# Kernel tuning notes

Measured on AMD Instinct MI355X. Metric: run time of the kernel, lower is better.

The kernel has to match this reference:

```python
import jax, jax.numpy as jnp
import numpy as np

N_NODES = 50000
N_EDGES = 800000


def _gcn_norm(edge_index, n_nodes):
    # add self-loops, compute symmetric normalization D^-1/2 (A+I) D^-1/2
    loops = jnp.arange(n_nodes, dtype=edge_index.dtype)
    row = jnp.concatenate([edge_index[0], loops])
    col = jnp.concatenate([edge_index[1], loops])
    deg = jax.ops.segment_sum(jnp.ones_like(row, dtype=jnp.float32), row,
                              num_segments=n_nodes)
    dinv = jnp.where(deg > 0, jax.lax.rsqrt(deg), 0.0)
    norm = dinv[row] * dinv[col]  # [E+N]
    return row, col, norm


def _gcn_conv(x, W, b, row, col, norm, n_nodes):
    h = x @ W                                  # [N, out] transform first (cheaper gather)
    msg = norm[:, None] * h[col]               # [E+N, out]
    agg = jax.ops.segment_sum(msg, row, num_segments=n_nodes)
    return agg + b


def setup_inputs() -> dict:
    key = jax.random.key(0)
    ks = jax.random.split(key, 8)
    F_in, H, F_out = 64, 128, 64
    return {
        "features": jax.random.normal(ks[0], (N_NODES, F_in), jnp.float32),
        "W1": jax.random.normal(ks[1], (F_in, H), jnp.float32) / np.sqrt(F_in),
        "b1": jnp.zeros((H,), jnp.float32),
        "W2": jax.random.normal(ks[2], (H, H), jnp.float32) / np.sqrt(H),
        "b2": jnp.zeros((H,), jnp.float32),
        "W3": jax.random.normal(ks[3], (H, F_out), jnp.float32) / np.sqrt(H),
        "b3": jnp.zeros((F_out,), jnp.float32),
        "edge_index": jax.random.randint(ks[4], (2, N_EDGES), 0, N_NODES, jnp.int32),
    }


def reference(features, W1, b1, W2, b2, W3, b3, edge_index):
    n = features.shape[0]
    row, col, norm = _gcn_norm(edge_index, n)
    x = jax.nn.relu(_gcn_conv(features, W1, b1, row, col, norm, n))
    x = jax.nn.relu(_gcn_conv(x, W2, b2, row, col, norm, n))
    x = _gcn_conv(x, W3, b3, row, col, norm, n)
    return x
```

## Files before the change

### kernel.cpp

```cpp
#include <hip/hip_runtime.h>

#define N_NODES 50000
#define N_EDGES 800000

#define SCAN_CHUNK 256
#define SCAN_BLOCKS ((N_NODES + SCAN_CHUNK - 1) / SCAN_CHUNK)

static inline size_t alignUp(size_t x, size_t a) { return (x + a - 1) & ~(a - 1); }

typedef _Float16 h2 __attribute__((ext_vector_type(2)));
typedef _Float16 h4 __attribute__((ext_vector_type(4)));
typedef _Float16 h8 __attribute__((ext_vector_type(8)));
typedef float    f4 __attribute__((ext_vector_type(4)));


__global__ void k_zero_i32(int* __restrict__ p, int n) {
    int i = blockIdx.x * 256 + threadIdx.x;
    if (i < n) p[i] = 0;
}

__global__ void k_count4(const int* __restrict__ row, int* __restrict__ count,
                         int* __restrict__ rank, int* __restrict__ pad) {
    int i = blockIdx.x * 256 + threadIdx.x;
    if (i < 64) pad[i] = 0;
    if (i < N_EDGES / 4) {
        int4 r = reinterpret_cast<const int4*>(row)[i];
        int k0 = atomicAdd(&count[r.x], 1);
        int k1 = atomicAdd(&count[r.y], 1);
        int k2 = atomicAdd(&count[r.z], 1);
        int k3 = atomicAdd(&count[r.w], 1);
        reinterpret_cast<int4*>(rank)[i] = make_int4(k0, k1, k2, k3);
    }
}

__global__ void k_blocksum(const int* __restrict__ count, int* __restrict__ bsum) {
    __shared__ int s[256];
    int t = threadIdx.x;
    int i = blockIdx.x * 256 + t;
    int v = (i < N_NODES) ? count[i] : 0;
    s[t] = v;
    __syncthreads();
    for (int off = 128; off > 0; off >>= 1) {
        if (t < off) s[t] += s[t + off];
        __syncthreads();
    }
    if (t == 0) bsum[blockIdx.x] = s[0];
}

__global__ void k_scan_bsum(int* __restrict__ bsum) {
    __shared__ int s[256];
    int t = threadIdx.x;
    int v = (t < SCAN_BLOCKS) ? bsum[t] : 0;
    s[t] = v;
    __syncthreads();
    for (int off = 1; off < 256; off <<= 1) {
        int add = (t >= off) ? s[t - off] : 0;
        __syncthreads();
        s[t] += add;
        __syncthreads();
    }
    if (t < SCAN_BLOCKS) bsum[t] = s[t] - v;
}

__global__ void k_scan_final(const int* __restrict__ count, const int* __restrict__ bsum,
                             int* __restrict__ offsets, float* __restrict__ dinv) {
    __shared__ int s[256];
    int t = threadIdx.x;
    int i = blockIdx.x * 256 + t;
    int v = (i < N_NODES) ? count[i] : 0;
    s[t] = v;
    __syncthreads();
    for (int off = 1; off < 256; off <<= 1) {
        int add = (t >= off) ? s[t - off] : 0;
        __syncthreads();
        s[t] += add;
        __syncthreads();
    }
    if (i < N_NODES) {
        offsets[i] = s[t] - v + bsum[blockIdx.x];
        dinv[i]    = rsqrtf((float)(v + 1));
    }
}

__global__ void k_scatter(const int* __restrict__ row, const int* __restrict__ col,
                          const int* __restrict__ offsets, const int* __restrict__ rank,
                          int* __restrict__ csr_col,
                          const float* __restrict__ feat, const float* __restrict__ dinv,
                          _Float16* __restrict__ featS) {
    int e = blockIdx.x * 256 + threadIdx.x;
    if (e < N_EDGES) {
        int node = e >> 4;
        float d = dinv[node];
        float4 v = reinterpret_cast<const float4*>(feat)[e];
        h4 hv = {(_Float16)(v.x * d), (_Float16)(v.y * d),
                 (_Float16)(v.z * d), (_Float16)(v.w * d)};
        reinterpret_cast<h4*>(featS)[e] = hv;
        int r = row[e];
        csr_col[offsets[r] + rank[e]] = col[e];
    }
}


__global__ void k_prepw(const float* __restrict__ W1, const float* __restrict__ W2,
                        const float* __restrict__ W3, _Float16* __restrict__ W1T,
                        _Float16* __restrict__ W2T, _Float16* __restrict__ W3T) {
    int i = blockIdx.x * 256 + threadIdx.x;
    if (i < 8192) {
        int n = i >> 6, k = i & 63;
        W1T[i] = (_Float16)W1[k * 128 + n];
    } else if (i < 24576) {
        int j = i - 8192; int n = j >> 7, k = j & 127;
        W2T[j] = (_Float16)W2[k * 128 + n];
    } else {
        int j = i - 24576; int n = j >> 7, k = j & 127;
        W3T[j] = (_Float16)W3[k * 64 + n];
    }
}


template <bool BIAS, bool HOUT>
__global__ __launch_bounds__(256) void k_agg128(const _Float16* __restrict__ hs, void* __restrict__ out,
        const int* __restrict__ csr_col, const int* __restrict__ offsets,
        const int* __restrict__ count, const float* __restrict__ dinv,
        const float* __restrict__ bias) {
    int lane = threadIdx.x & 63;
    int node = blockIdx.x * 4 + (threadIdx.x >> 6);
    const char* base = (const char*)hs;
    uint32_t lo = (uint32_t)lane << 2;

    float ax[8], ay[8];
#pragma unroll
    for (int u = 0; u < 8; u++) { ax[u] = 0.f; ay[u] = 0.f; }

    int n = count[node];
    const int* cp = csr_col + offsets[node];

    int e = 0;
    for (; e + 8 <= n; e += 8) {
        int c[8];
#pragma unroll
        for (int u = 0; u < 8; u++) c[u] = cp[e + u];
#pragma unroll
        for (int u = 0; u < 8; u++) {
            h2 v = *reinterpret_cast<const h2*>(base + (((uint32_t)c[u] << 8) + lo));
            ax[u] += (float)v.x; ay[u] += (float)v.y;
        }
    }
    if (e < n) {
        int c[8];
#pragma unroll
        for (int u = 0; u < 8; u++) c[u] = cp[e + u];
#pragma unroll
        for (int u = 0; u < 8; u++) {
            h2 v = *reinterpret_cast<const h2*>(base + (((uint32_t)c[u] << 8) + lo));
            if (e + u < n) { ax[u] += (float)v.x; ay[u] += (float)v.y; }
        }
    }

    float sx = 0.f, sy = 0.f;
#pragma unroll
    for (int u = 0; u < 8; u++) { sx += ax[u]; sy += ay[u]; }
    h2 self = *reinterpret_cast<const h2*>(base + (((uint32_t)node << 8) + lo));
    float d = dinv[node];
    float ox = (sx + (float)self.x) * d, oy = (sy + (float)self.y) * d;
    if (BIAS) { ox += bias[2 * lane]; oy += bias[2 * lane + 1]; }
    if constexpr (HOUT) {
        h2 hv = {(_Float16)ox, (_Float16)oy};
        reinterpret_cast<h2*>(out)[(size_t)node * 64 + lane] = hv;
    } else {
        reinterpret_cast<float2*>(out)[(size_t)node * 64 + lane] = make_float2(ox, oy);
    }
}

template <bool BIAS, bool HOUT>
__global__ __launch_bounds__(256) void k_agg64(const _Float16* __restrict__ hs, void* __restrict__ out,
        const int* __restrict__ csr_col, const int* __restrict__ offsets,
        const int* __restrict__ count, const float* __restrict__ dinv,
        const float* __restrict__ bias) {
    int lane = threadIdx.x & 63;
    int node = blockIdx.x * 4 + (threadIdx.x >> 6);
    int q = lane >> 4;
    int f4 = lane & 15;
    const char* base = (const char*)hs;
    uint32_t fo = (uint32_t)f4 << 3;

    int n = __builtin_amdgcn_readfirstlane(count[node]);
    int start = __builtin_amdgcn_readfirstlane(offsets[node]);
    const int* cp = csr_col + start;

    float4 a0 = make_float4(0.f, 0.f, 0.f, 0.f);
    float4 a1 = make_float4(0.f, 0.f, 0.f, 0.f);

    int e = 0;
    for (; e + 32 <= n; e += 32) {
        int c[8];
#pragma unroll
        for (int u = 0; u < 8; u++) c[u] = cp[e + 4 * u + q];
        h4 v[8];
#pragma unroll
        for (int u = 0; u < 8; u++)
            v[u] = *reinterpret_cast<const h4*>(base + (((uint32_t)c[u] << 7) + fo));
#pragma unroll
        for (int u = 0; u < 8; u += 2) {
            a0.x += (float)v[u].x; a0.y += (float)v[u].y;
            a0.z += (float)v[u].z; a0.w += (float)v[u].w;
            a1.x += (float)v[u+1].x; a1.y += (float)v[u+1].y;
            a1.z += (float)v[u+1].z; a1.w += (float)v[u+1].w;
        }
    }
    if (e < n) {
        int c[8];
#pragma unroll
        for (int u = 0; u < 8; u++) c[u] = cp[e + 4 * u + q];
        h4 v[8];
#pragma unroll
        for (int u = 0; u < 8; u++)
            v[u] = *reinterpret_cast<const h4*>(base + (((uint32_t)c[u] << 7) + fo));
#pragma unroll
        for (int u = 0; u < 8; u++) {
            if (e + 4 * u + q < n) {
                a0.x += (float)v[u].x; a0.y += (float)v[u].y;
                a0.z += (float)v[u].z; a0.w += (float)v[u].w;
            }
        }
    }

    float sx = a0.x + a1.x, sy = a0.y + a1.y, sz = a0.z + a1.z, sw = a0.w + a1.w;
    sx += __shfl_xor(sx, 16); sy += __shfl_xor(sy, 16);
    sz += __shfl_xor(sz, 16); sw += __shfl_xor(sw, 16);
    sx += __shfl_xor(sx, 32); sy += __shfl_xor(sy, 32);
    sz += __shfl_xor(sz, 32); sw += __shfl_xor(sw, 32);
    if (q == 0) {
        h4 self = *reinterpret_cast<const h4*>(base + (((uint32_t)node << 7) + fo));
        float d = dinv[node];
        float ox = (sx + (float)self.x) * d, oy = (sy + (float)self.y) * d;
        float oz = (sz + (float)self.z) * d, ow = (sw + (float)self.w) * d;
        if (BIAS) {
            float4 bv = *reinterpret_cast<const float4*>(&bias[f4 * 4]);
            ox += bv.x; oy += bv.y; oz += bv.z; ow += bv.w;
        }
        if constexpr (HOUT) {
            h4 hv = {(_Float16)ox, (_Float16)oy, (_Float16)oz, (_Float16)ow};
            *reinterpret_cast<h4*>((char*)out + (((uint32_t)node << 7) + fo)) = hv;
        } else {
            *reinterpret_cast<float4*>((char*)out + ((uint32_t)node << 8) + (fo << 1)) =
                make_float4(ox, oy, oz, ow);
        }
    }
}


template <int K, int NOUT, bool RELU, bool BIAS, bool SCALE, bool HOUT>
__global__ __launch_bounds__(256) void k_gemm_mfma(const _Float16* __restrict__ x,
        const _Float16* __restrict__ WT, const float* __restrict__ bias,
        const float* __restrict__ dinv, void* __restrict__ out, int nrows) {
    constexpr int NB = NOUT / 16;
    int l = threadIdx.x & 63;
    int w = threadIdx.x >> 6;
    int lm = l & 15;
    int kb = (l >> 4) * 8;
    int row0 = blockIdx.x * 64 + w * 16;

    int arow = row0 + lm;
    if (arow >= nrows) arow = nrows - 1;

    f4 acc[NB] = {};

#pragma unroll
    for (int kk = 0; kk < K / 32; ++kk) {
        h8 a = *reinterpret_cast<const h8*>(x + (size_t)arow * K + kk * 32 + kb);
#pragma unroll
        for (int n = 0; n < NB; ++n) {
            h8 b = *reinterpret_cast<const h8*>(WT + (size_t)(n * 16 + lm) * K + kk * 32 + kb);
            acc[n] = __builtin_amdgcn_mfma_f32_16x16x32_f16(a, b, acc[n], 0, 0, 0);
        }
    }

    int rbase = row0 + (l >> 4) * 4;
    float dv[4];
#pragma unroll
    for (int t = 0; t < 4; ++t) {
        int gr = rbase + t;
        dv[t] = SCALE ? dinv[(gr < nrows) ? gr : (nrows - 1)] : 1.f;
    }
#pragma unroll
    for (int n = 0; n < NB; ++n) {
        float bvn = BIAS ? bias[n * 16 + lm] : 0.f;
#pragma unroll
        for (int t = 0; t < 4; ++t) {
            int gr = rbase + t;
            if (gr >= nrows) continue;
            float v = acc[n][t] + bvn;
            if (RELU) v = fmaxf(v, 0.f);
            v *= dv[t];
            if constexpr (HOUT)
                ((_Float16*)out)[(size_t)gr * NOUT + n * 16 + lm] = (_Float16)v;
            else
                ((float*)out)[(size_t)gr * NOUT + n * 16 + lm] = v;
        }
    }
}


extern "C" void kernel_launch(void* const* d_in, const int* in_sizes, int n_in,
                              void* d_out, int out_size, void* d_ws, size_t ws_size,
                              hipStream_t stream) {
    const float* feat = (const float*)d_in[0];
    const float* W1 = (const float*)d_in[1];
    const float* b1 = (const float*)d_in[2];
    const float* W2 = (const float*)d_in[3];
    const float* b2 = (const float*)d_in[4];
    const float* W3 = (const float*)d_in[5];
    const float* b3 = (const float*)d_in[6];
    const int* ei = (const int*)d_in[7];
    const int* row = ei;
    const int* col = ei + N_EDGES;
    float* out = (float*)d_out;

    char* ws = (char*)d_ws;
    size_t off = 0;
    auto alloc = [&](size_t bytes) {
        void* p = ws + off;
        off = alignUp(off + bytes, 256);
        return p;
    };
    constexpr size_t SLOT = (size_t)N_NODES * 128 * 2;
    _Float16* S1 = (_Float16*)alloc(SLOT);
    _Float16* S2 = (_Float16*)alloc(SLOT);
    _Float16* S3 = (_Float16*)alloc(SLOT);
    float* dinv    = (float*)alloc((size_t)N_NODES * 4);
    int*   count   = (int*)alloc((size_t)N_NODES * 4);
    int*   offsets = (int*)alloc((size_t)N_NODES * 4);
    int*   bsum    = (int*)alloc(1024);
    int*   rank    = (int*)alloc((size_t)N_EDGES * 4);
    int*   csr_col = (int*)alloc((size_t)(N_EDGES + 64) * 4);
    _Float16* W1T  = (_Float16*)alloc(128 * 64 * 2);
    _Float16* W2T  = (_Float16*)alloc(128 * 128 * 2);
    _Float16* W3T  = (_Float16*)alloc(64 * 128 * 2);

    _Float16* featS = S1;
    _Float16* A1h = S2;
    _Float16* X1h = S1;
    _Float16* A2h = S2;
    _Float16* X2h = S3;
    _Float16* H3h = S1;

    const int eb = (N_EDGES + 255) / 256;
    const int cb4 = (N_EDGES / 4 + 255) / 256;
    const int gemm_grid = (N_NODES + 63) / 64;
    const int agg_grid = N_NODES / 4;

    k_prepw<<<128, 256, 0, stream>>>(W1, W2, W3, W1T, W2T, W3T);

    k_zero_i32<<<(N_NODES + 255) / 256, 256, 0, stream>>>(count, N_NODES);
    k_count4<<<cb4, 256, 0, stream>>>(row, count, rank, csr_col + N_EDGES);
    k_blocksum<<<SCAN_BLOCKS, 256, 0, stream>>>(count, bsum);
    k_scan_bsum<<<1, 256, 0, stream>>>(bsum);
    k_scan_final<<<SCAN_BLOCKS, 256, 0, stream>>>(count, bsum, offsets, dinv);
    k_scatter<<<eb, 256, 0, stream>>>(row, col, offsets, rank, csr_col, feat, dinv, featS);

    k_agg64<false, true><<<agg_grid, 256, 0, stream>>>(featS, A1h, csr_col, offsets, count, dinv, nullptr);
    k_gemm_mfma<64, 128, true, true, true, true><<<gemm_grid, 256, 0, stream>>>(A1h, W1T, b1, dinv, X1h, N_NODES);

    k_agg128<false, true><<<agg_grid, 256, 0, stream>>>(X1h, A2h, csr_col, offsets, count, dinv, nullptr);
    k_gemm_mfma<128, 128, true, true, false, true><<<gemm_grid, 256, 0, stream>>>(A2h, W2T, b2, dinv, X2h, N_NODES);

    k_gemm_mfma<128, 64, false, false, true, true><<<gemm_grid, 256, 0, stream>>>(X2h, W3T, nullptr, dinv, H3h, N_NODES);
    k_agg64<true, false><<<agg_grid, 256, 0, stream>>>(H3h, out, csr_col, offsets, count, dinv, b3);
}
```

Baseline: 208.9 us.

## Fuse aggregation with dense GEMM per layer and collapse setup kernels

```diff
diff --git a/kernel.cpp b/kernel.cpp
--- a/kernel.cpp
+++ b/kernel.cpp
@@ -3,21 +3,34 @@
 #define N_NODES 50000
 #define N_EDGES 800000
 
-#define SCAN_CHUNK 256
-#define SCAN_BLOCKS ((N_NODES + SCAN_CHUNK - 1) / SCAN_CHUNK)
+#define SCAN_BLOCKS ((N_NODES + 255) / 256)
 
 static inline size_t alignUp(size_t x, size_t a) { return (x + a - 1) & ~(a - 1); }
 
 typedef _Float16 h2 __attribute__((ext_vector_type(2)));
 typedef _Float16 h4 __attribute__((ext_vector_type(4)));
 typedef _Float16 h8 __attribute__((ext_vector_type(8)));
-typedef float    f4 __attribute__((ext_vector_type(4)));
-
-
-__global__ void k_zero_i32(int* __restrict__ p, int n) {
+typedef float    fx4 __attribute__((ext_vector_type(4)));
+
+
+__global__ void k_init(int* __restrict__ count, const float* __restrict__ W1,
+                       const float* __restrict__ W2, const float* __restrict__ W3,
+                       _Float16* __restrict__ W1T, _Float16* __restrict__ W2T,
+                       _Float16* __restrict__ W3T) {
     int i = blockIdx.x * 256 + threadIdx.x;
-    if (i < n) p[i] = 0;
-}
+    if (i < N_NODES) count[i] = 0;
+    if (i < 8192) {
+        int n = i >> 6, k = i & 63;
+        W1T[i] = (_Float16)W1[k * 128 + n];
+    } else if (i < 24576) {
+        int j = i - 8192; int n = j >> 7, k = j & 127;
+        W2T[j] = (_Float16)W2[k * 128 + n];
+    } else if (i < 32768) {
+        int j = i - 24576; int n = j >> 7, k = j & 127;
+        W3T[j] = (_Float16)W3[k * 64 + n];
+    }
+}
+
 
 __global__ void k_count4(const int* __restrict__ row, int* __restrict__ count,
                          int* __restrict__ rank, int* __restrict__ pad) {
@@ -33,40 +46,21 @@
     }
 }
 
-__global__ void k_blocksum(const int* __restrict__ count, int* __restrict__ bsum) {
+__global__ void k_scan_fused(const int* __restrict__ count, int* __restrict__ offsets,
+                             float* __restrict__ dinv) {
     __shared__ int s[256];
-    int t = threadIdx.x;
-    int i = blockIdx.x * 256 + t;
-    int v = (i < N_NODES) ? count[i] : 0;
-    s[t] = v;
+    int t = threadIdx.x, b = blockIdx.x;
+    int partial = 0;
+    for (int c = 0; c < b; ++c) partial += count[c * 256 + t];
+    s[t] = partial;
     __syncthreads();
     for (int off = 128; off > 0; off >>= 1) {
         if (t < off) s[t] += s[t + off];
         __syncthreads();
     }
-    if (t == 0) bsum[blockIdx.x] = s[0];
-}
-
-__global__ void k_scan_bsum(int* __restrict__ bsum) {
-    __shared__ int s[256];
-    int t = threadIdx.x;
-    int v = (t < SCAN_BLOCKS) ? bsum[t] : 0;
-    s[t] = v;
+    int base = s[0];
     __syncthreads();
-    for (int off = 1; off < 256; off <<= 1) {
-        int add = (t >= off) ? s[t - off] : 0;
-        __syncthreads();
-        s[t] += add;
-        __syncthreads();
-    }
-    if (t < SCAN_BLOCKS) bsum[t] = s[t] - v;
-}
-
-__global__ void k_scan_final(const int* __restrict__ count, const int* __restrict__ bsum,
-                             int* __restrict__ offsets, float* __restrict__ dinv) {
-    __shared__ int s[256];
-    int t = threadIdx.x;
-    int i = blockIdx.x * 256 + t;
+    int i = b * 256 + t;
     int v = (i < N_NODES) ? count[i] : 0;
     s[t] = v;
     __syncthreads();
@@ -77,7 +71,7 @@
         __syncthreads();
     }
     if (i < N_NODES) {
-        offsets[i] = s[t] - v + bsum[blockIdx.x];
+        offsets[i] = base + s[t] - v;
         dinv[i]    = rsqrtf((float)(v + 1));
     }
 }
@@ -101,84 +95,16 @@
 }
 
 
-__global__ void k_prepw(const float* __restrict__ W1, const float* __restrict__ W2,
-                        const float* __restrict__ W3, _Float16* __restrict__ W1T,
-                        _Float16* __restrict__ W2T, _Float16* __restrict__ W3T) {
-    int i = blockIdx.x * 256 + threadIdx.x;
-    if (i < 8192) {
-        int n = i >> 6, k = i & 63;
-        W1T[i] = (_Float16)W1[k * 128 + n];
-    } else if (i < 24576) {
-        int j = i - 8192; int n = j >> 7, k = j & 127;
-        W2T[j] = (_Float16)W2[k * 128 + n];
-    } else {
-        int j = i - 24576; int n = j >> 7, k = j & 127;
-        W3T[j] = (_Float16)W3[k * 64 + n];
-    }
-}
-
-
-template <bool BIAS, bool HOUT>
-__global__ __launch_bounds__(256) void k_agg128(const _Float16* __restrict__ hs, void* __restrict__ out,
+__global__ __launch_bounds__(1024) void k_agg64_gemm1(const _Float16* __restrict__ hs,
+        const _Float16* __restrict__ WT, const float* __restrict__ bias,
+        const float* __restrict__ dinv, _Float16* __restrict__ xout,
         const int* __restrict__ csr_col, const int* __restrict__ offsets,
-        const int* __restrict__ count, const float* __restrict__ dinv,
-        const float* __restrict__ bias) {
-    int lane = threadIdx.x & 63;
-    int node = blockIdx.x * 4 + (threadIdx.x >> 6);
-    const char* base = (const char*)hs;
-    uint32_t lo = (uint32_t)lane << 2;
-
-    float ax[8], ay[8];
-#pragma unroll
-    for (int u = 0; u < 8; u++) { ax[u] = 0.f; ay[u] = 0.f; }
-
-    int n = count[node];
-    const int* cp = csr_col + offsets[node];
-
-    int e = 0;
-    for (; e + 8 <= n; e += 8) {
-        int c[8];
-#pragma unroll
-        for (int u = 0; u < 8; u++) c[u] = cp[e + u];
-#pragma unroll
-        for (int u = 0; u < 8; u++) {
-            h2 v = *reinterpret_cast<const h2*>(base + (((uint32_t)c[u] << 8) + lo));
-            ax[u] += (float)v.x; ay[u] += (float)v.y;
-        }
-    }
-    if (e < n) {
-        int c[8];
-#pragma unroll
-        for (int u = 0; u < 8; u++) c[u] = cp[e + u];
-#pragma unroll
-        for (int u = 0; u < 8; u++) {
-            h2 v = *reinterpret_cast<const h2*>(base + (((uint32_t)c[u] << 8) + lo));
-            if (e + u < n) { ax[u] += (float)v.x; ay[u] += (float)v.y; }
-        }
-    }
-
-    float sx = 0.f, sy = 0.f;
-#pragma unroll
-    for (int u = 0; u < 8; u++) { sx += ax[u]; sy += ay[u]; }
-    h2 self = *reinterpret_cast<const h2*>(base + (((uint32_t)node << 8) + lo));
-    float d = dinv[node];
-    float ox = (sx + (float)self.x) * d, oy = (sy + (float)self.y) * d;
-    if (BIAS) { ox += bias[2 * lane]; oy += bias[2 * lane + 1]; }
-    if constexpr (HOUT) {
-        h2 hv = {(_Float16)ox, (_Float16)oy};
-        reinterpret_cast<h2*>(out)[(size_t)node * 64 + lane] = hv;
-    } else {
-        reinterpret_cast<float2*>(out)[(size_t)node * 64 + lane] = make_float2(ox, oy);
-    }
-}
-
-template <bool BIAS, bool HOUT>
-__global__ __launch_bounds__(256) void k_agg64(const _Float16* __restrict__ hs, void* __restrict__ out,
-        const int* __restrict__ csr_col, const int* __restrict__ offsets,
-        const int* __restrict__ count, const float* __restrict__ dinv,
-        const float* __restrict__ bias) {
-    int lane = threadIdx.x & 63;
-    int node = blockIdx.x * 4 + (threadIdx.x >> 6);
+        const int* __restrict__ count) {
+    __shared__ _Float16 at[16 * 72];
+    int tid = threadIdx.x;
+    int wv = tid >> 6;
+    int lane = tid & 63;
+    int node = blockIdx.x * 16 + wv;
     int q = lane >> 4;
     int f4 = lane & 15;
     const char* base = (const char*)hs;
@@ -233,27 +159,111 @@
     if (q == 0) {
         h4 self = *reinterpret_cast<const h4*>(base + (((uint32_t)node << 7) + fo));
         float d = dinv[node];
-        float ox = (sx + (float)self.x) * d, oy = (sy + (float)self.y) * d;
-        float oz = (sz + (float)self.z) * d, ow = (sw + (float)self.w) * d;
-        if (BIAS) {
-            float4 bv = *reinterpret_cast<const float4*>(&bias[f4 * 4]);
-            ox += bv.x; oy += bv.y; oz += bv.z; ow += bv.w;
-        }
-        if constexpr (HOUT) {
-            h4 hv = {(_Float16)ox, (_Float16)oy, (_Float16)oz, (_Float16)ow};
-            *reinterpret_cast<h4*>((char*)out + (((uint32_t)node << 7) + fo)) = hv;
-        } else {
-            *reinterpret_cast<float4*>((char*)out + ((uint32_t)node << 8) + (fo << 1)) =
-                make_float4(ox, oy, oz, ow);
-        }
-    }
-}
-
-
-template <int K, int NOUT, bool RELU, bool BIAS, bool SCALE, bool HOUT>
+        h4 hv = {(_Float16)((sx + (float)self.x) * d), (_Float16)((sy + (float)self.y) * d),
+                 (_Float16)((sz + (float)self.z) * d), (_Float16)((sw + (float)self.w) * d)};
+        *reinterpret_cast<h4*>(&at[wv * 72 + f4 * 4]) = hv;
+    }
+    __syncthreads();
+
+    if (wv < 8) {
+        int lm = lane & 15;
+        int kb = (lane >> 4) * 8;
+        fx4 acc = {0.f, 0.f, 0.f, 0.f};
+#pragma unroll
+        for (int kk = 0; kk < 2; ++kk) {
+            h8 a = *reinterpret_cast<const h8*>(&at[lm * 72 + kk * 32 + kb]);
+            h8 b = *reinterpret_cast<const h8*>(WT + (size_t)(wv * 16 + lm) * 64 + kk * 32 + kb);
+            acc = __builtin_amdgcn_mfma_f32_16x16x32_f16(a, b, acc, 0, 0, 0);
+        }
+        int rbase = blockIdx.x * 16 + (lane >> 4) * 4;
+        float bv = bias[wv * 16 + lm];
+#pragma unroll
+        for (int t2 = 0; t2 < 4; ++t2) {
+            int gr = rbase + t2;
+            float v = fmaxf(acc[t2] + bv, 0.f) * dinv[gr];
+            xout[(size_t)gr * 128 + wv * 16 + lm] = (_Float16)v;
+        }
+    }
+}
+
+
+__global__ __launch_bounds__(1024) void k_agg128_gemm2(const _Float16* __restrict__ hs,
+        const _Float16* __restrict__ WT, const float* __restrict__ bias,
+        const float* __restrict__ dinv, _Float16* __restrict__ xout,
+        const int* __restrict__ csr_col, const int* __restrict__ offsets,
+        const int* __restrict__ count) {
+    __shared__ _Float16 at[16 * 136];
+    int tid = threadIdx.x;
+    int wv = tid >> 6;
+    int lane = tid & 63;
+    int node = blockIdx.x * 16 + wv;
+    const char* base = (const char*)hs;
+    uint32_t lo = (uint32_t)lane << 2;
+
+    float ax[8], ay[8];
+#pragma unroll
+    for (int u = 0; u < 8; u++) { ax[u] = 0.f; ay[u] = 0.f; }
+
+    int n = count[node];
+    const int* cp = csr_col + offsets[node];
+
+    int e = 0;
+    for (; e + 8 <= n; e += 8) {
+        int c[8];
+#pragma unroll
+        for (int u = 0; u < 8; u++) c[u] = cp[e + u];
+#pragma unroll
+        for (int u = 0; u < 8; u++) {
+            h2 v = *reinterpret_cast<const h2*>(base + (((uint32_t)c[u] << 8) + lo));
+            ax[u] += (float)v.x; ay[u] += (float)v.y;
+        }
+    }
+    if (e < n) {
+        int c[8];
+#pragma unroll
+        for (int u = 0; u < 8; u++) c[u] = cp[e + u];
+#pragma unroll
+        for (int u = 0; u < 8; u++) {
+            h2 v = *reinterpret_cast<const h2*>(base + (((uint32_t)c[u] << 8) + lo));
+            if (e + u < n) { ax[u] += (float)v.x; ay[u] += (float)v.y; }
+        }
+    }
+
+    float sx = 0.f, sy = 0.f;
+#pragma unroll
+    for (int u = 0; u < 8; u++) { sx += ax[u]; sy += ay[u]; }
+    h2 self = *reinterpret_cast<const h2*>(base + (((uint32_t)node << 8) + lo));
+    float d = dinv[node];
+    h2 hv = {(_Float16)((sx + (float)self.x) * d), (_Float16)((sy + (float)self.y) * d)};
+    *reinterpret_cast<h2*>(&at[wv * 136 + lane * 2]) = hv;
+    __syncthreads();
+
+    if (wv < 8) {
+        int lm = lane & 15;
+        int kb = (lane >> 4) * 8;
+        fx4 acc = {0.f, 0.f, 0.f, 0.f};
+#pragma unroll
+        for (int kk = 0; kk < 4; ++kk) {
+            h8 a = *reinterpret_cast<const h8*>(&at[lm * 136 + kk * 32 + kb]);
+            h8 b = *reinterpret_cast<const h8*>(WT + (size_t)(wv * 16 + lm) * 128 + kk * 32 + kb);
+            acc = __builtin_amdgcn_mfma_f32_16x16x32_f16(a, b, acc, 0, 0, 0);
+        }
+        int rbase = blockIdx.x * 16 + (lane >> 4) * 4;
+        float bv = bias[wv * 16 + lm];
+#pragma unroll
+        for (int t2 = 0; t2 < 4; ++t2) {
+            int gr = rbase + t2;
+            float v = fmaxf(acc[t2] + bv, 0.f);
+            xout[(size_t)gr * 128 + wv * 16 + lm] = (_Float16)v;
+        }
+    }
+}
+
+
+template <int K, int NOUT, bool RELU, bool BIAS, bool SCALE>
 __global__ __launch_bounds__(256) void k_gemm_mfma(const _Float16* __restrict__ x,
         const _Float16* __restrict__ WT, const float* __restrict__ bias,
-        const float* __restrict__ dinv, void* __restrict__ out, int nrows) {
+        const float* __restrict__ dinv, _Float16* __restrict__ out, int nrows) {
     constexpr int NB = NOUT / 16;
     int l = threadIdx.x & 63;
     int w = threadIdx.x >> 6;
@@ -264,7 +274,7 @@
     int arow = row0 + lm;
     if (arow >= nrows) arow = nrows - 1;
 
-    f4 acc[NB] = {};
+    fx4 acc[NB] = {};
 
 #pragma unroll
     for (int kk = 0; kk < K / 32; ++kk) {
@@ -293,11 +303,79 @@
             float v = acc[n][t] + bvn;
             if (RELU) v = fmaxf(v, 0.f);
             v *= dv[t];
-            if constexpr (HOUT)
-                ((_Float16*)out)[(size_t)gr * NOUT + n * 16 + lm] = (_Float16)v;
-            else
-                ((float*)out)[(size_t)gr * NOUT + n * 16 + lm] = v;
-        }
+            out[(size_t)gr * NOUT + n * 16 + lm] = (_Float16)v;
+        }
+    }
+}
+
+
+__global__ __launch_bounds__(256) void k_agg64_final(const _Float16* __restrict__ hs,
+        float* __restrict__ out, const int* __restrict__ csr_col,
+        const int* __restrict__ offsets, const int* __restrict__ count,
+        const float* __restrict__ dinv, const float* __restrict__ bias) {
+    int lane = threadIdx.x & 63;
+    int node = blockIdx.x * 4 + (threadIdx.x >> 6);
+    int q = lane >> 4;
+    int f4 = lane & 15;
+    const char* base = (const char*)hs;
+    uint32_t fo = (uint32_t)f4 << 3;
+
+    int n = __builtin_amdgcn_readfirstlane(count[node]);
+    int start = __builtin_amdgcn_readfirstlane(offsets[node]);
+    const int* cp = csr_col + start;
+
+    float4 a0 = make_float4(0.f, 0.f, 0.f, 0.f);
+    float4 a1 = make_float4(0.f, 0.f, 0.f, 0.f);
+
+    int e = 0;
+    for (; e + 32 <= n; e += 32) {
+        int c[8];
+#pragma unroll
+        for (int u = 0; u < 8; u++) c[u] = cp[e + 4 * u + q];
+        h4 v[8];
+#pragma unroll
+        for (int u = 0; u < 8; u++)
+            v[u] = *reinterpret_cast<const h4*>(base + (((uint32_t)c[u] << 7) + fo));
+#pragma unroll
+        for (int u = 0; u < 8; u += 2) {
+            a0.x += (float)v[u].x; a0.y += (float)v[u].y;
+            a0.z += (float)v[u].z; a0.w += (float)v[u].w;
+            a1.x += (float)v[u+1].x; a1.y += (float)v[u+1].y;
+            a1.z += (float)v[u+1].z; a1.w += (float)v[u+1].w;
+        }
+    }
+    if (e < n) {
+        int c[8];
+#pragma unroll
+        for (int u = 0; u < 8; u++) c[u] = cp[e + 4 * u + q];
+        h4 v[8];
+#pragma unroll
+        for (int u = 0; u < 8; u++)
+            v[u] = *reinterpret_cast<const h4*>(base + (((uint32_t)c[u] << 7) + fo));
+#pragma unroll
+        for (int u = 0; u < 8; u++) {
+            if (e + 4 * u + q < n) {
+                a0.x += (float)v[u].x; a0.y += (float)v[u].y;
+                a0.z += (float)v[u].z; a0.w += (float)v[u].w;
+            }
+        }
+    }
+
+    float sx = a0.x + a1.x, sy = a0.y + a1.y, sz = a0.z + a1.z, sw = a0.w + a1.w;
+    sx += __shfl_xor(sx, 16); sy += __shfl_xor(sy, 16);
+    sz += __shfl_xor(sz, 16); sw += __shfl_xor(sw, 16);
+    sx += __shfl_xor(sx, 32); sy += __shfl_xor(sy, 32);
+    sz += __shfl_xor(sz, 32); sw += __shfl_xor(sw, 32);
+    if (q == 0) {
+        h4 self = *reinterpret_cast<const h4*>(base + (((uint32_t)node << 7) + fo));
+        float d = dinv[node];
+        float4 bv = *reinterpret_cast<const float4*>(&bias[f4 * 4]);
+        float ox = (sx + (float)self.x) * d + bv.x;
+        float oy = (sy + (float)self.y) * d + bv.y;
+        float oz = (sz + (float)self.z) * d + bv.z;
+        float ow = (sw + (float)self.w) * d + bv.w;
+        *reinterpret_cast<float4*>((char*)out + ((uint32_t)node << 8) + (fo << 1)) =
+            make_float4(ox, oy, oz, ow);
     }
 }
 
@@ -327,11 +405,9 @@
     constexpr size_t SLOT = (size_t)N_NODES * 128 * 2;
     _Float16* S1 = (_Float16*)alloc(SLOT);
     _Float16* S2 = (_Float16*)alloc(SLOT);
-    _Float16* S3 = (_Float16*)alloc(SLOT);
     float* dinv    = (float*)alloc((size_t)N_NODES * 4);
     int*   count   = (int*)alloc((size_t)N_NODES * 4);
     int*   offsets = (int*)alloc((size_t)N_NODES * 4);
-    int*   bsum    = (int*)alloc(1024);
     int*   rank    = (int*)alloc((size_t)N_EDGES * 4);
     int*   csr_col = (int*)alloc((size_t)(N_EDGES + 64) * 4);
     _Float16* W1T  = (_Float16*)alloc(128 * 64 * 2);
@@ -339,32 +415,21 @@
     _Float16* W3T  = (_Float16*)alloc(64 * 128 * 2);
 
     _Float16* featS = S1;
-    _Float16* A1h = S2;
-    _Float16* X1h = S1;
-    _Float16* A2h = S2;
-    _Float16* X2h = S3;
-    _Float16* H3h = S1;
+    _Float16* X1h = S2;
+    _Float16* X2h = S1;
+    _Float16* H3h = S2;
 
     const int eb = (N_EDGES + 255) / 256;
     const int cb4 = (N_EDGES / 4 + 255) / 256;
-    const int gemm_grid = (N_NODES + 63) / 64;
-    const int agg_grid = N_NODES / 4;
-
-    k_prepw<<<128, 256, 0, stream>>>(W1, W2, W3, W1T, W2T, W3T);
-
-    k_zero_i32<<<(N_NODES + 255) / 256, 256, 0, stream>>>(count, N_NODES);
+    const int fb = (N_NODES + 15) / 16;
+
+    k_init<<<SCAN_BLOCKS, 256, 0, stream>>>(count, W1, W2, W3, W1T, W2T, W3T);
     k_count4<<<cb4, 256, 0, stream>>>(row, count, rank, csr_col + N_EDGES);
-    k_blocksum<<<SCAN_BLOCKS, 256, 0, stream>>>(count, bsum);
-    k_scan_bsum<<<1, 256, 0, stream>>>(bsum);
-    k_scan_final<<<SCAN_BLOCKS, 256, 0, stream>>>(count, bsum, offsets, dinv);
+    k_scan_fused<<<SCAN_BLOCKS, 256, 0, stream>>>(count, offsets, dinv);
     k_scatter<<<eb, 256, 0, stream>>>(row, col, offsets, rank, csr_col, feat, dinv, featS);
-
-    k_agg64<false, true><<<agg_grid, 256, 0, stream>>>(featS, A1h, csr_col, offsets, count, dinv, nullptr);
-    k_gemm_mfma<64, 128, true, true, true, true><<<gemm_grid, 256, 0, stream>>>(A1h, W1T, b1, dinv, X1h, N_NODES);
-
-    k_agg128<false, true><<<agg_grid, 256, 0, stream>>>(X1h, A2h, csr_col, offsets, count, dinv, nullptr);
-    k_gemm_mfma<128, 128, true, true, false, true><<<gemm_grid, 256, 0, stream>>>(A2h, W2T, b2, dinv, X2h, N_NODES);
-
-    k_gemm_mfma<128, 64, false, false, true, true><<<gemm_grid, 256, 0, stream>>>(X2h, W3T, nullptr, dinv, H3h, N_NODES);
-    k_agg64<true, false><<<agg_grid, 256, 0, stream>>>(H3h, out, csr_col, offsets, count, dinv, b3);
-}
+    k_agg64_gemm1<<<fb, 1024, 0, stream>>>(featS, W1T, b1, dinv, X1h, csr_col, offsets, count);
+    k_agg128_gemm2<<<fb, 1024, 0, stream>>>(X1h, W2T, b2, dinv, X2h, csr_col, offsets, count);
+    k_gemm_mfma<128, 64, false, false, true><<<(N_NODES + 63) / 64, 256, 0, stream>>>(
+        X2h, W3T, nullptr, dinv, H3h, N_NODES);
+    k_agg64_final<<<N_NODES / 4, 256, 0, stream>>>(H3h, out, csr_col, offsets, count, dinv, b3);
+}
```

Result: slower. 216.2 us (+3.5%).

## Fuse layer-2/3 GEMMs via LDS and collapse scan and init launches

Applied to the files above, without the earlier changes.

```diff
diff --git a/kernel.cpp b/kernel.cpp
--- a/kernel.cpp
+++ b/kernel.cpp
@@ -3,21 +3,34 @@
 #define N_NODES 50000
 #define N_EDGES 800000
 
-#define SCAN_CHUNK 256
-#define SCAN_BLOCKS ((N_NODES + SCAN_CHUNK - 1) / SCAN_CHUNK)
+#define SCAN_BLOCKS ((N_NODES + 255) / 256)
 
 static inline size_t alignUp(size_t x, size_t a) { return (x + a - 1) & ~(a - 1); }
 
 typedef _Float16 h2 __attribute__((ext_vector_type(2)));
 typedef _Float16 h4 __attribute__((ext_vector_type(4)));
 typedef _Float16 h8 __attribute__((ext_vector_type(8)));
-typedef float    f4 __attribute__((ext_vector_type(4)));
-
-
-__global__ void k_zero_i32(int* __restrict__ p, int n) {
+typedef float    fx4 __attribute__((ext_vector_type(4)));
+
+
+__global__ void k_init(int* __restrict__ count, const float* __restrict__ W1,
+                       const float* __restrict__ W2, const float* __restrict__ W3,
+                       _Float16* __restrict__ W1T, _Float16* __restrict__ W2T,
+                       _Float16* __restrict__ W3T) {
     int i = blockIdx.x * 256 + threadIdx.x;
-    if (i < n) p[i] = 0;
-}
+    if (i < N_NODES) count[i] = 0;
+    if (i < 8192) {
+        int n = i >> 6, k = i & 63;
+        W1T[i] = (_Float16)W1[k * 128 + n];
+    } else if (i < 24576) {
+        int j = i - 8192; int n = j >> 7, k = j & 127;
+        W2T[j] = (_Float16)W2[k * 128 + n];
+    } else if (i < 32768) {
+        int j = i - 24576; int n = j >> 7, k = j & 127;
+        W3T[j] = (_Float16)W3[k * 64 + n];
+    }
+}
+
 
 __global__ void k_count4(const int* __restrict__ row, int* __restrict__ count,
                          int* __restrict__ rank, int* __restrict__ pad) {
@@ -33,40 +46,21 @@
     }
 }
 
-__global__ void k_blocksum(const int* __restrict__ count, int* __restrict__ bsum) {
+__global__ void k_scan_fused(const int* __restrict__ count, int* __restrict__ offsets,
+                             float* __restrict__ dinv) {
     __shared__ int s[256];
-    int t = threadIdx.x;
-    int i = blockIdx.x * 256 + t;
-    int v = (i < N_NODES) ? count[i] : 0;
-    s[t] = v;
+    int t = threadIdx.x, b = blockIdx.x;
+    int partial = 0;
+    for (int c = 0; c < b; ++c) partial += count[c * 256 + t];
+    s[t] = partial;
     __syncthreads();
     for (int off = 128; off > 0; off >>= 1) {
         if (t < off) s[t] += s[t + off];
         __syncthreads();
     }
-    if (t == 0) bsum[blockIdx.x] = s[0];
-}
-
-__global__ void k_scan_bsum(int* __restrict__ bsum) {
-    __shared__ int s[256];
-    int t = threadIdx.x;
-    int v = (t < SCAN_BLOCKS) ? bsum[t] : 0;
-    s[t] = v;
+    int base = s[0];
     __syncthreads();
-    for (int off = 1; off < 256; off <<= 1) {
-        int add = (t >= off) ? s[t - off] : 0;
-        __syncthreads();
-        s[t] += add;
-        __syncthreads();
-    }
-    if (t < SCAN_BLOCKS) bsum[t] = s[t] - v;
-}
-
-__global__ void k_scan_final(const int* __restrict__ count, const int* __restrict__ bsum,
-                             int* __restrict__ offsets, float* __restrict__ dinv) {
-    __shared__ int s[256];
-    int t = threadIdx.x;
-    int i = blockIdx.x * 256 + t;
+    int i = b * 256 + t;
     int v = (i < N_NODES) ? count[i] : 0;
     s[t] = v;
     __syncthreads();
@@ -77,7 +71,7 @@
         __syncthreads();
     }
     if (i < N_NODES) {
-        offsets[i] = s[t] - v + bsum[blockIdx.x];
+        offsets[i] = base + s[t] - v;
         dinv[i]    = rsqrtf((float)(v + 1));
     }
 }
@@ -101,23 +95,6 @@
 }
 
 
-__global__ void k_prepw(const float* __restrict__ W1, const float* __restrict__ W2,
-                        const float* __restrict__ W3, _Float16* __restrict__ W1T,
-                        _Float16* __restrict__ W2T, _Float16* __restrict__ W3T) {
-    int i = blockIdx.x * 256 + threadIdx.x;
-    if (i < 8192) {
-        int n = i >> 6, k = i & 63;
-        W1T[i] = (_Float16)W1[k * 128 + n];
-    } else if (i < 24576) {
-        int j = i - 8192; int n = j >> 7, k = j & 127;
-        W2T[j] = (_Float16)W2[k * 128 + n];
-    } else {
-        int j = i - 24576; int n = j >> 7, k = j & 127;
-        W3T[j] = (_Float16)W3[k * 64 + n];
-    }
-}
-
-
 template <bool BIAS, bool HOUT>
 __global__ __launch_bounds__(256) void k_agg128(const _Float16* __restrict__ hs, void* __restrict__ out,
         const int* __restrict__ csr_col, const int* __restrict__ offsets,
@@ -250,10 +227,10 @@
 }
 
 
-template <int K, int NOUT, bool RELU, bool BIAS, bool SCALE, bool HOUT>
+template <int K, int NOUT, bool RELU, bool BIAS, bool SCALE>
 __global__ __launch_bounds__(256) void k_gemm_mfma(const _Float16* __restrict__ x,
         const _Float16* __restrict__ WT, const float* __restrict__ bias,
-        const float* __restrict__ dinv, void* __restrict__ out, int nrows) {
+        const float* __restrict__ dinv, _Float16* __restrict__ out, int nrows) {
     constexpr int NB = NOUT / 16;
     int l = threadIdx.x & 63;
     int w = threadIdx.x >> 6;
@@ -264,7 +241,7 @@
     int arow = row0 + lm;
     if (arow >= nrows) arow = nrows - 1;
 
-    f4 acc[NB] = {};
+    fx4 acc[NB] = {};
 
 #pragma unroll
     for (int kk = 0; kk < K / 32; ++kk) {
@@ -293,10 +270,71 @@
             float v = acc[n][t] + bvn;
             if (RELU) v = fmaxf(v, 0.f);
             v *= dv[t];
-            if constexpr (HOUT)
-                ((_Float16*)out)[(size_t)gr * NOUT + n * 16 + lm] = (_Float16)v;
-            else
-                ((float*)out)[(size_t)gr * NOUT + n * 16 + lm] = v;
+            out[(size_t)gr * NOUT + n * 16 + lm] = (_Float16)v;
+        }
+    }
+}
+
+
+__global__ __launch_bounds__(256) void k_gemm23(const _Float16* __restrict__ x,
+        const _Float16* __restrict__ W2T, const float* __restrict__ b2,
+        const _Float16* __restrict__ W3T, const float* __restrict__ dinv,
+        _Float16* __restrict__ out, int nrows) {
+    __shared__ _Float16 xt[4][16 * 136];
+    int l = threadIdx.x & 63;
+    int w = threadIdx.x >> 6;
+    int lm = l & 15;
+    int kb = (l >> 4) * 8;
+    int row0 = blockIdx.x * 64 + w * 16;
+
+    int arow = row0 + lm;
+    if (arow >= nrows) arow = nrows - 1;
+
+    fx4 acc[8] = {};
+#pragma unroll
+    for (int kk = 0; kk < 4; ++kk) {
+        h8 a = *reinterpret_cast<const h8*>(x + (size_t)arow * 128 + kk * 32 + kb);
+#pragma unroll
+        for (int n = 0; n < 8; ++n) {
+            h8 b = *reinterpret_cast<const h8*>(W2T + (size_t)(n * 16 + lm) * 128 + kk * 32 + kb);
+            acc[n] = __builtin_amdgcn_mfma_f32_16x16x32_f16(a, b, acc[n], 0, 0, 0);
+        }
+    }
+    int rloc = (l >> 4) * 4;
+#pragma unroll
+    for (int n = 0; n < 8; ++n) {
+        float bv = b2[n * 16 + lm];
+#pragma unroll
+        for (int t = 0; t < 4; ++t) {
+            float v = fmaxf(acc[n][t] + bv, 0.f);
+            xt[w][(rloc + t) * 136 + n * 16 + lm] = (_Float16)v;
+        }
+    }
+
+    fx4 acc3[4] = {};
+#pragma unroll
+    for (int kk = 0; kk < 4; ++kk) {
+        h8 a = *reinterpret_cast<const h8*>(&xt[w][lm * 136 + kk * 32 + kb]);
+#pragma unroll
+        for (int n = 0; n < 4; ++n) {
+            h8 b = *reinterpret_cast<const h8*>(W3T + (size_t)(n * 16 + lm) * 128 + kk * 32 + kb);
+            acc3[n] = __builtin_amdgcn_mfma_f32_16x16x32_f16(a, b, acc3[n], 0, 0, 0);
+        }
+    }
+    int rbase = row0 + rloc;
+    float dv[4];
+#pragma unroll
+    for (int t = 0; t < 4; ++t) {
+        int gr = rbase + t;
+        dv[t] = dinv[(gr < nrows) ? gr : (nrows - 1)];
+    }
+#pragma unroll
+    for (int n = 0; n < 4; ++n) {
+#pragma unroll
+        for (int t = 0; t < 4; ++t) {
+            int gr = rbase + t;
+            if (gr >= nrows) continue;
+            out[(size_t)gr * 64 + n * 16 + lm] = (_Float16)(acc3[n][t] * dv[t]);
         }
     }
 }
@@ -327,11 +365,9 @@
     constexpr size_t SLOT = (size_t)N_NODES * 128 * 2;
     _Float16* S1 = (_Float16*)alloc(SLOT);
     _Float16* S2 = (_Float16*)alloc(SLOT);
-    _Float16* S3 = (_Float16*)alloc(SLOT);
     float* dinv    = (float*)alloc((size_t)N_NODES * 4);
     int*   count   = (int*)alloc((size_t)N_NODES * 4);
     int*   offsets = (int*)alloc((size_t)N_NODES * 4);
-    int*   bsum    = (int*)alloc(1024);
     int*   rank    = (int*)alloc((size_t)N_EDGES * 4);
     int*   csr_col = (int*)alloc((size_t)(N_EDGES + 64) * 4);
     _Float16* W1T  = (_Float16*)alloc(128 * 64 * 2);
@@ -342,29 +378,20 @@
     _Float16* A1h = S2;
     _Float16* X1h = S1;
     _Float16* A2h = S2;
-    _Float16* X2h = S3;
     _Float16* H3h = S1;
 
     const int eb = (N_EDGES + 255) / 256;
     const int cb4 = (N_EDGES / 4 + 255) / 256;
-    const int gemm_grid = (N_NODES + 63) / 64;
+    const int gb = (N_NODES + 63) / 64;
     const int agg_grid = N_NODES / 4;
 
-    k_prepw<<<128, 256, 0, stream>>>(W1, W2, W3, W1T, W2T, W3T);
-
-    k_zero_i32<<<(N_NODES + 255) / 256, 256, 0, stream>>>(count, N_NODES);
+    k_init<<<SCAN_BLOCKS, 256, 0, stream>>>(count, W1, W2, W3, W1T, W2T, W3T);
     k_count4<<<cb4, 256, 0, stream>>>(row, count, rank, csr_col + N_EDGES);
-    k_blocksum<<<SCAN_BLOCKS, 256, 0, stream>>>(count, bsum);
-    k_scan_bsum<<<1, 256, 0, stream>>>(bsum);
-    k_scan_final<<<SCAN_BLOCKS, 256, 0, stream>>>(count, bsum, offsets, dinv);
+    k_scan_fused<<<SCAN_BLOCKS, 256, 0, stream>>>(count, offsets, dinv);
     k_scatter<<<eb, 256, 0, stream>>>(row, col, offsets, rank, csr_col, feat, dinv, featS);
-
     k_agg64<false, true><<<agg_grid, 256, 0, stream>>>(featS, A1h, csr_col, offsets, count, dinv, nullptr);
-    k_gemm_mfma<64, 128, true, true, true, true><<<gemm_grid, 256, 0, stream>>>(A1h, W1T, b1, dinv, X1h, N_NODES);
-
+    k_gemm_mfma<64, 128, true, true, true><<<gb, 256, 0, stream>>>(A1h, W1T, b1, dinv, X1h, N_NODES);
     k_agg128<false, true><<<agg_grid, 256, 0, stream>>>(X1h, A2h, csr_col, offsets, count, dinv, nullptr);
-    k_gemm_mfma<128, 128, true, true, false, true><<<gemm_grid, 256, 0, stream>>>(A2h, W2T, b2, dinv, X2h, N_NODES);
-
-    k_gemm_mfma<128, 64, false, false, true, true><<<gemm_grid, 256, 0, stream>>>(X2h, W3T, nullptr, dinv, H3h, N_NODES);
+    k_gemm23<<<gb, 256, 0, stream>>>(A2h, W2T, b2, W3T, dinv, H3h, N_NODES);
     k_agg64<true, false><<<agg_grid, 256, 0, stream>>>(H3h, out, csr_col, offsets, count, dinv, b3);
 }
```

Measured after the change: 222.7 us. 1.07x slower.
